# Optimization experiments

Hardware: AMD Instinct MI355X
Metric: run time of the kernel (lower is better)

Reference implementation:

```python
import jax, jax.numpy as jnp
import numpy as np

N = 100000
E = 1600000
F_IN = 32
HID = 16


def _sage_conv(x, src, dst, W_l, b_l, W_r):
    # PyG SAGEConv (aggr='mean', normalize=False, root_weight=True):
    #   out = lin_l(mean_{j in N(i)} x_j) + lin_r(x_i)
    # lin_l has bias, lin_r has no bias.
    n = x.shape[0]
    msg_sum = jax.ops.segment_sum(x[src], dst, num_segments=n)          # [N, d]
    deg = jax.ops.segment_sum(jnp.ones_like(dst, dtype=x.dtype), dst, num_segments=n)
    agg = msg_sum / jnp.maximum(deg, 1.0)[:, None]                      # mean, 0 for isolated nodes
    return agg @ W_l.T + b_l + x @ W_r.T


def setup_inputs() -> dict:
    key = jax.random.key(0)
    ks = jax.random.split(key, 8)
    x = jax.random.normal(ks[0], (N, F_IN), dtype=jnp.float32)
    edge_index = jax.random.randint(ks[1], (1, 2, E), 0, N, dtype=jnp.int64)
    s1 = 1.0 / np.sqrt(F_IN)
    s2 = 1.0 / np.sqrt(HID)
    W1_l = jax.random.uniform(ks[2], (HID, F_IN), jnp.float32, -s1, s1)
    b1_l = jax.random.uniform(ks[3], (HID,), jnp.float32, -s1, s1)
    W1_r = jax.random.uniform(ks[4], (HID, F_IN), jnp.float32, -s1, s1)
    W2_l = jax.random.uniform(ks[5], (F_IN, HID), jnp.float32, -s2, s2)
    b2_l = jax.random.uniform(ks[6], (F_IN,), jnp.float32, -s2, s2)
    W2_r = jax.random.uniform(ks[7], (F_IN, HID), jnp.float32, -s2, s2)
    return {"x": x, "edge_index": edge_index, "W1_l": W1_l, "b1_l": b1_l,
            "W1_r": W1_r, "W2_l": W2_l, "b2_l": b2_l, "W2_r": W2_r}


def reference(x, edge_index, W1_l, b1_l, W1_r, W2_l, b2_l, W2_r):
    ei = jnp.squeeze(edge_index, axis=0)  # [2, E]
    src, dst = ei[0], ei[1]
    h = jax.nn.relu(_sage_conv(x, src, dst, W1_l, b1_l, W1_r))
    out = _sage_conv(h, src, dst, W2_l, b2_l, W2_r)
    return out
```

## Files before the change

### kernel.cpp

```cpp
#include <hip/hip_runtime.h>

#define F_IN 32
#define HID 16
#define BSHIFT 6
#define BNODES (1 << BSHIFT)
#define CAP 1440
#define NBINS 2048
#define CHUNK 8192
#define SRCM 0x1FFFFu
#define WS2 17

__device__ __forceinline__ void add4(float4& a, const float4& b) {
    a.x += b.x; a.y += b.y; a.z += b.z; a.w += b.w;
}
__device__ __forceinline__ unsigned pack2(float a, float b) {
    unsigned ua = __float_as_uint(a);
    unsigned ub = __float_as_uint(b);
    ua = (ua + 0x7FFFu + ((ua >> 16) & 1u)) >> 16;
    ub = (ub + 0x7FFFu + ((ub >> 16) & 1u)) >> 16;
    return ua | (ub << 16);
}
__device__ __forceinline__ float lo2f(unsigned u) { return __uint_as_float(u << 16); }
__device__ __forceinline__ float hi2f(unsigned u) { return __uint_as_float(u & 0xFFFF0000u); }
__device__ __forceinline__ float4 unp(uint2 v) {
    return make_float4(lo2f(v.x), hi2f(v.x), lo2f(v.y), hi2f(v.y));
}

__global__ void __launch_bounds__(256) k_pre(const float* __restrict__ x,
                                             const float* __restrict__ W1_l,
                                             const float* __restrict__ b1,
                                             const float* __restrict__ W1_r,
                                             unsigned* __restrict__ y1b,
                                             float* __restrict__ y1r,
                                             const int* __restrict__ ei,
                                             int* __restrict__ bucketCursor,
                                             unsigned* __restrict__ bucketBuf,
                                             int N, int E, int nodeBlocks) {
    __shared__ int cnt[NBINS];
    __shared__ int runBase[NBINS];
    __shared__ float Wa[HID * F_IN];
    __shared__ float Wb[HID * F_IN];
    __shared__ float bb[HID];
    int tid = threadIdx.x;

    if ((int)blockIdx.x < nodeBlocks) {
        for (int i = tid; i < HID * F_IN; i += 256) { Wa[i] = W1_l[i]; Wb[i] = W1_r[i]; }
        if (tid < HID) bb[tid] = b1[tid];
        __syncthreads();
        int node = blockIdx.x * 256 + tid;
        if (node >= N) return;
        float xr[F_IN];
        const float4* xp = (const float4*)(x + (size_t)node * F_IN);
#pragma unroll
        for (int i = 0; i < F_IN / 4; i++) {
            float4 v = xp[i];
            xr[4 * i + 0] = v.x; xr[4 * i + 1] = v.y;
            xr[4 * i + 2] = v.z; xr[4 * i + 3] = v.w;
        }
        float a[HID];
#pragma unroll
        for (int o = 0; o < HID; o++) {
            float s = 0.f;
#pragma unroll
            for (int k = 0; k < F_IN; k++) s += xr[k] * Wa[o * F_IN + k];
            a[o] = s;
        }
        uint4* yp = (uint4*)(y1b + (size_t)node * 8);
        yp[0] = make_uint4(pack2(a[0], a[1]), pack2(a[2], a[3]),
                           pack2(a[4], a[5]), pack2(a[6], a[7]));
        yp[1] = make_uint4(pack2(a[8], a[9]), pack2(a[10], a[11]),
                           pack2(a[12], a[13]), pack2(a[14], a[15]));
#pragma unroll
        for (int o = 0; o < HID; o++) {
            float s = bb[o];
#pragma unroll
            for (int k = 0; k < F_IN; k++) s += xr[k] * Wb[o * F_IN + k];
            a[o] = s;
        }
        float4* rp = (float4*)(y1r + (size_t)node * HID);
        rp[0] = make_float4(a[0], a[1], a[2], a[3]);
        rp[1] = make_float4(a[4], a[5], a[6], a[7]);
        rp[2] = make_float4(a[8], a[9], a[10], a[11]);
        rp[3] = make_float4(a[12], a[13], a[14], a[15]);
        return;
    }

    int pb = blockIdx.x - nodeBlocks;
    int e0 = pb * CHUNK;
    int e1 = min(e0 + CHUNK, E);
    int n4 = (e1 - e0) >> 2;
    const int4* dst4 = (const int4*)(ei + E + e0);
    const int4* src4 = (const int4*)(ei + e0);

#pragma unroll
    for (int i = 0; i < NBINS / 256; i++) cnt[tid + 256 * i] = 0;
    __syncthreads();
    for (int i = tid; i < n4; i += 256) {
        int4 d = dst4[i];
        atomicAdd(&cnt[d.x >> BSHIFT], 1);
        atomicAdd(&cnt[d.y >> BSHIFT], 1);
        atomicAdd(&cnt[d.z >> BSHIFT], 1);
        atomicAdd(&cnt[d.w >> BSHIFT], 1);
    }
    __syncthreads();
#pragma unroll
    for (int i = 0; i < NBINS / 256; i++) {
        int b = tid + 256 * i;
        int c = cnt[b];
        runBase[b] = c ? atomicAdd(&bucketCursor[b], c) : 0;
        cnt[b] = 0;
    }
    __syncthreads();
    for (int i = tid; i < n4; i += 256) {
        int4 d = dst4[i];
        int4 s = src4[i];
        {
            int b = d.x >> BSHIFT;
            int pos = runBase[b] + atomicAdd(&cnt[b], 1);
            if (pos < CAP)
                bucketBuf[(size_t)b * CAP + pos] = ((unsigned)(d.x & (BNODES - 1)) << 17) | (unsigned)s.x;
        }
        {
            int b = d.y >> BSHIFT;
            int pos = runBase[b] + atomicAdd(&cnt[b], 1);
            if (pos < CAP)
                bucketBuf[(size_t)b * CAP + pos] = ((unsigned)(d.y & (BNODES - 1)) << 17) | (unsigned)s.y;
        }
        {
            int b = d.z >> BSHIFT;
            int pos = runBase[b] + atomicAdd(&cnt[b], 1);
            if (pos < CAP)
                bucketBuf[(size_t)b * CAP + pos] = ((unsigned)(d.z & (BNODES - 1)) << 17) | (unsigned)s.z;
        }
        {
            int b = d.w >> BSHIFT;
            int pos = runBase[b] + atomicAdd(&cnt[b], 1);
            if (pos < CAP)
                bucketBuf[(size_t)b * CAP + pos] = ((unsigned)(d.w & (BNODES - 1)) << 17) | (unsigned)s.w;
        }
    }
}

__global__ void __launch_bounds__(256) k_agg1f(const unsigned* __restrict__ y1b,
                                               const float* __restrict__ y1r,
                                               unsigned* __restrict__ bucketBuf,
                                               const int* __restrict__ bucketCursor,
                                               unsigned* __restrict__ hb,
                                               int* __restrict__ meta, int N) {
    __shared__ __align__(16) unsigned sA[CAP];
    __shared__ __align__(16) unsigned sB[CAP];
    __shared__ int hist[BNODES];
    __shared__ int scn[BNODES];
    __shared__ int cur[BNODES];
    int tid = threadIdx.x, b = blockIdx.x;

    if (tid < BNODES) hist[tid] = 0;
    int nRec = min(bucketCursor[b], CAP);
    unsigned* buf = bucketBuf + (size_t)b * CAP;
    int n4s = (nRec + 3) >> 2;
    for (int i = tid; i < n4s; i += 256)
        ((uint4*)sA)[i] = ((const uint4*)buf)[i];
    __syncthreads();
    for (int i = tid; i < nRec; i += 256) atomicAdd(&hist[sA[i] >> 17], 1);
    __syncthreads();
    if (tid < BNODES) scn[tid] = hist[tid];
    __syncthreads();
    for (int off = 1; off < BNODES; off <<= 1) {
        int v = (tid < BNODES && tid >= off) ? scn[tid - off] : 0;
        __syncthreads();
        if (tid < BNODES && tid >= off) scn[tid] += v;
        __syncthreads();
    }
    if (tid < BNODES) cur[tid] = scn[tid] - hist[tid];
    __syncthreads();
    for (int i = tid; i < nRec; i += 256) {
        unsigned r = sA[i];
        int pos = atomicAdd(&cur[r >> 17], 1);
        sB[pos] = r & SRCM;
    }
    __syncthreads();

    for (int i = tid; i < n4s; i += 256)
        ((uint4*)buf)[i] = ((const uint4*)sB)[i];
    if (tid < BNODES) {
        meta[(size_t)b * 128 + tid] = scn[tid] - hist[tid];
        meta[(size_t)b * 128 + BNODES + tid] = scn[tid];
    }

    const uint2* yv = (const uint2*)y1b;
    {
        int nl = tid >> 2, c = tid & 3;
        int node = b * BNODES + nl;
        if (node < N) {
            int start = scn[nl] - hist[nl];
            int dg = hist[nl];
            int jend = start + dg;
            float4 a0 = make_float4(0, 0, 0, 0), a1 = a0;
            int j = start;
            for (; j + 4 <= jend; j += 4) {
                unsigned s0 = sB[j], s1 = sB[j + 1], s2 = sB[j + 2], s3 = sB[j + 3];
                uint2 v0 = yv[(size_t)s0 * 4 + c];
                uint2 v1 = yv[(size_t)s1 * 4 + c];
                uint2 v2 = yv[(size_t)s2 * 4 + c];
                uint2 v3 = yv[(size_t)s3 * 4 + c];
                add4(a0, unp(v0)); add4(a1, unp(v1));
                add4(a0, unp(v2)); add4(a1, unp(v3));
            }
            for (; j < jend; j++) {
                uint2 v = yv[(size_t)sB[j] * 4 + c];
                add4(a0, unp(v));
            }
            add4(a0, a1);
            float inv = 1.0f / (float)(dg > 0 ? dg : 1);
            float4 r4 = ((const float4*)(y1r + (size_t)node * HID))[c];
            float o0 = fmaxf(a0.x * inv + r4.x, 0.0f);
            float o1 = fmaxf(a0.y * inv + r4.y, 0.0f);
            float o2 = fmaxf(a0.z * inv + r4.z, 0.0f);
            float o3 = fmaxf(a0.w * inv + r4.w, 0.0f);
            ((uint2*)hb)[(size_t)node * 4 + c] = make_uint2(pack2(o0, o1), pack2(o2, o3));
        }
    }
}

__global__ void __launch_bounds__(256) k_l2f(const unsigned* __restrict__ hb,
                                             const unsigned* __restrict__ bucketBuf,
                                             const int* __restrict__ bucketCursor,
                                             const int* __restrict__ meta,
                                             const float* __restrict__ W2_l,
                                             const float* __restrict__ b2,
                                             const float* __restrict__ W2_r,
                                             float* __restrict__ out, int N) {
    __shared__ __align__(16) unsigned sB[CAP];
    __shared__ int s0[BNODES];
    __shared__ int s1[BNODES];
    __shared__ float mm[BNODES * (HID + 1)];
    __shared__ float Wl[F_IN * WS2];
    __shared__ float Wr[F_IN * WS2];
    __shared__ float bs[F_IN];
    int tid = threadIdx.x, b = blockIdx.x;

    for (int i = tid; i < F_IN * HID; i += 256) {
        int r = i >> 4, q = i & 15;
        Wl[r * WS2 + q] = W2_l[i];
        Wr[r * WS2 + q] = W2_r[i];
    }
    if (tid < F_IN) bs[tid] = b2[tid];
    if (tid < BNODES) {
        s0[tid] = meta[(size_t)b * 128 + tid];
        s1[tid] = meta[(size_t)b * 128 + BNODES + tid];
    }
    int nRec = min(bucketCursor[b], CAP);
    const uint4* bv = (const uint4*)(bucketBuf + (size_t)b * CAP);
    int n4s = (nRec + 3) >> 2;
    for (int i = tid; i < n4s; i += 256) ((uint4*)sB)[i] = bv[i];
    __syncthreads();

    const uint2* hv = (const uint2*)hb;
    {
        int nl = tid >> 2, c = tid & 3;
        int node = b * BNODES + nl;
        if (node < N) {
            int start = s0[nl];
            int jend = s1[nl];
            int dg = jend - start;
            float4 a0 = make_float4(0, 0, 0, 0), a1 = a0;
            int j = start;
            for (; j + 4 <= jend; j += 4) {
                unsigned v0i = sB[j], v1i = sB[j + 1], v2i = sB[j + 2], v3i = sB[j + 3];
                uint2 v0 = hv[(size_t)v0i * 4 + c];
                uint2 v1 = hv[(size_t)v1i * 4 + c];
                uint2 v2 = hv[(size_t)v2i * 4 + c];
                uint2 v3 = hv[(size_t)v3i * 4 + c];
                add4(a0, unp(v0)); add4(a1, unp(v1));
                add4(a0, unp(v2)); add4(a1, unp(v3));
            }
            for (; j < jend; j++) {
                uint2 v = hv[(size_t)sB[j] * 4 + c];
                add4(a0, unp(v));
            }
            add4(a0, a1);
            float inv = 1.0f / (float)(dg > 0 ? dg : 1);
            mm[nl * (HID + 1) + c * 4 + 0] = a0.x * inv;
            mm[nl * (HID + 1) + c * 4 + 1] = a0.y * inv;
            mm[nl * (HID + 1) + c * 4 + 2] = a0.z * inv;
            mm[nl * (HID + 1) + c * 4 + 3] = a0.w * inv;
        }
    }
    __syncthreads();

    {
        int nl = tid >> 2, c = tid & 3;
        int node = b * BNODES + nl;
        if (node >= N) return;

        float m[HID];
#pragma unroll
        for (int k = 0; k < HID; k++) m[k] = mm[nl * (HID + 1) + k];

        float hr[HID];
        const uint4* hp = (const uint4*)(hb + (size_t)node * 8);
        uint4 u0 = hp[0], u1 = hp[1];
        hr[0] = lo2f(u0.x); hr[1] = hi2f(u0.x); hr[2] = lo2f(u0.y); hr[3] = hi2f(u0.y);
        hr[4] = lo2f(u0.z); hr[5] = hi2f(u0.z); hr[6] = lo2f(u0.w); hr[7] = hi2f(u0.w);
        hr[8] = lo2f(u1.x); hr[9] = hi2f(u1.x); hr[10] = lo2f(u1.y); hr[11] = hi2f(u1.y);
        hr[12] = lo2f(u1.z); hr[13] = hi2f(u1.z); hr[14] = lo2f(u1.w); hr[15] = hi2f(u1.w);

        float a[8];
#pragma unroll
        for (int jj = 0; jj < 8; jj++) {
            int o = c * 8 + jj;
            float s = bs[o];
#pragma unroll
            for (int k = 0; k < HID; k++)
                s += m[k] * Wl[o * WS2 + k] + hr[k] * Wr[o * WS2 + k];
            a[jj] = s;
        }
        float4* op = (float4*)(out + (size_t)node * F_IN + c * 8);
        op[0] = make_float4(a[0], a[1], a[2], a[3]);
        op[1] = make_float4(a[4], a[5], a[6], a[7]);
    }
}

extern "C" void kernel_launch(void* const* d_in, const int* in_sizes, int n_in,
                              void* d_out, int out_size, void* d_ws, size_t ws_size,
                              hipStream_t stream) {
    const float* x    = (const float*)d_in[0];
    const int*   ei   = (const int*)d_in[1];
    const float* W1_l = (const float*)d_in[2];
    const float* b1   = (const float*)d_in[3];
    const float* W1_r = (const float*)d_in[4];
    const float* W2_l = (const float*)d_in[5];
    const float* b2   = (const float*)d_in[6];
    const float* W2_r = (const float*)d_in[7];
    float* out = (float*)d_out;

    const int N = in_sizes[0] / F_IN;
    const int E = in_sizes[1] / 2;
    const int nbuckets = (N + BNODES - 1) >> BSHIFT;

    int* bucketCursor = (int*)d_ws;
    unsigned* bucketBuf = (unsigned*)(bucketCursor + NBINS);
    unsigned* y1b = bucketBuf + (size_t)nbuckets * CAP;
    unsigned* hb  = y1b + (size_t)N * 8;
    int* meta = (int*)(hb + (size_t)N * 8);
    float* y1r = (float*)(meta + (size_t)nbuckets * 128);

    hipMemsetAsync(bucketCursor, 0, NBINS * sizeof(int), stream);

    const int nodeBlocks = (N + 255) / 256;
    const int partBlocks = (E + CHUNK - 1) / CHUNK;

    k_pre<<<nodeBlocks + partBlocks, 256, 0, stream>>>(x, W1_l, b1, W1_r,
                                                       y1b, y1r, ei,
                                                       bucketCursor, bucketBuf,
                                                       N, E, nodeBlocks);
    k_agg1f<<<nbuckets, 256, 0, stream>>>(y1b, y1r, bucketBuf, bucketCursor,
                                          hb, meta, N);
    k_l2f<<<nbuckets, 256, 0, stream>>>(hb, bucketBuf, bucketCursor, meta,
                                        W2_l, b2, W2_r, out, N);
}
```

Before: 147.3 us.

## Replace shared-memory binning with direct global atomics per edge in bucketing pass

```diff
diff --git a/kernel.cpp b/kernel.cpp
--- a/kernel.cpp
+++ b/kernel.cpp
@@ -6,7 +6,7 @@
 #define BNODES (1 << BSHIFT)
 #define CAP 1440
 #define NBINS 2048
-#define CHUNK 8192
+#define CHUNK 2048
 #define SRCM 0x1FFFFu
 #define WS2 17
 
@@ -36,14 +36,12 @@
                                              int* __restrict__ bucketCursor,
                                              unsigned* __restrict__ bucketBuf,
                                              int N, int E, int nodeBlocks) {
-    __shared__ int cnt[NBINS];
-    __shared__ int runBase[NBINS];
-    __shared__ float Wa[HID * F_IN];
-    __shared__ float Wb[HID * F_IN];
-    __shared__ float bb[HID];
     int tid = threadIdx.x;
 
     if ((int)blockIdx.x < nodeBlocks) {
+        __shared__ float Wa[HID * F_IN];
+        __shared__ float Wb[HID * F_IN];
+        __shared__ float bb[HID];
         for (int i = tid; i < HID * F_IN; i += 256) { Wa[i] = W1_l[i]; Wb[i] = W1_r[i]; }
         if (tid < HID) bb[tid] = b1[tid];
         __syncthreads();
@@ -92,52 +90,23 @@
     const int4* dst4 = (const int4*)(ei + E + e0);
     const int4* src4 = (const int4*)(ei + e0);
 
-#pragma unroll
-    for (int i = 0; i < NBINS / 256; i++) cnt[tid + 256 * i] = 0;
-    __syncthreads();
-    for (int i = tid; i < n4; i += 256) {
-        int4 d = dst4[i];
-        atomicAdd(&cnt[d.x >> BSHIFT], 1);
-        atomicAdd(&cnt[d.y >> BSHIFT], 1);
-        atomicAdd(&cnt[d.z >> BSHIFT], 1);
-        atomicAdd(&cnt[d.w >> BSHIFT], 1);
-    }
-    __syncthreads();
-#pragma unroll
-    for (int i = 0; i < NBINS / 256; i++) {
-        int b = tid + 256 * i;
-        int c = cnt[b];
-        runBase[b] = c ? atomicAdd(&bucketCursor[b], c) : 0;
-        cnt[b] = 0;
-    }
-    __syncthreads();
     for (int i = tid; i < n4; i += 256) {
         int4 d = dst4[i];
         int4 s = src4[i];
-        {
-            int b = d.x >> BSHIFT;
-            int pos = runBase[b] + atomicAdd(&cnt[b], 1);
-            if (pos < CAP)
-                bucketBuf[(size_t)b * CAP + pos] = ((unsigned)(d.x & (BNODES - 1)) << 17) | (unsigned)s.x;
-        }
-        {
-            int b = d.y >> BSHIFT;
-            int pos = runBase[b] + atomicAdd(&cnt[b], 1);
-            if (pos < CAP)
-                bucketBuf[(size_t)b * CAP + pos] = ((unsigned)(d.y & (BNODES - 1)) << 17) | (unsigned)s.y;
-        }
-        {
-            int b = d.z >> BSHIFT;
-            int pos = runBase[b] + atomicAdd(&cnt[b], 1);
-            if (pos < CAP)
-                bucketBuf[(size_t)b * CAP + pos] = ((unsigned)(d.z & (BNODES - 1)) << 17) | (unsigned)s.z;
-        }
-        {
-            int b = d.w >> BSHIFT;
-            int pos = runBase[b] + atomicAdd(&cnt[b], 1);
-            if (pos < CAP)
-                bucketBuf[(size_t)b * CAP + pos] = ((unsigned)(d.w & (BNODES - 1)) << 17) | (unsigned)s.w;
-        }
+        int b0 = d.x >> BSHIFT, b1_ = d.y >> BSHIFT;
+        int b2_ = d.z >> BSHIFT, b3 = d.w >> BSHIFT;
+        int p0 = atomicAdd(&bucketCursor[b0], 1);
+        int p1 = atomicAdd(&bucketCursor[b1_], 1);
+        int p2 = atomicAdd(&bucketCursor[b2_], 1);
+        int p3 = atomicAdd(&bucketCursor[b3], 1);
+        if (p0 < CAP)
+            bucketBuf[(size_t)b0 * CAP + p0] = ((unsigned)(d.x & (BNODES - 1)) << 17) | (unsigned)s.x;
+        if (p1 < CAP)
+            bucketBuf[(size_t)b1_ * CAP + p1] = ((unsigned)(d.y & (BNODES - 1)) << 17) | (unsigned)s.y;
+        if (p2 < CAP)
+            bucketBuf[(size_t)b2_ * CAP + p2] = ((unsigned)(d.z & (BNODES - 1)) << 17) | (unsigned)s.z;
+        if (p3 < CAP)
+            bucketBuf[(size_t)b3 * CAP + p3] = ((unsigned)(d.w & (BNODES - 1)) << 17) | (unsigned)s.w;
     }
 }
 
```

Measured after the change: 362.9 us. 146% more time.

## Double bucket size to 128 nodes and gather 16-byte rows with 2 threads per node

Applied to the files above, without the earlier changes.

```diff
diff --git a/kernel.cpp b/kernel.cpp
--- a/kernel.cpp
+++ b/kernel.cpp
@@ -2,10 +2,10 @@
 
 #define F_IN 32
 #define HID 16
-#define BSHIFT 6
+#define BSHIFT 7
 #define BNODES (1 << BSHIFT)
-#define CAP 1440
-#define NBINS 2048
+#define CAP 2560
+#define NBINS 1024
 #define CHUNK 8192
 #define SRCM 0x1FFFFu
 #define WS2 17
@@ -22,8 +22,11 @@
 }
 __device__ __forceinline__ float lo2f(unsigned u) { return __uint_as_float(u << 16); }
 __device__ __forceinline__ float hi2f(unsigned u) { return __uint_as_float(u & 0xFFFF0000u); }
-__device__ __forceinline__ float4 unp(uint2 v) {
+__device__ __forceinline__ float4 unpLo(uint4 v) {
     return make_float4(lo2f(v.x), hi2f(v.x), lo2f(v.y), hi2f(v.y));
+}
+__device__ __forceinline__ float4 unpHi(uint4 v) {
+    return make_float4(lo2f(v.z), hi2f(v.z), lo2f(v.w), hi2f(v.w));
 }
 
 __global__ void __launch_bounds__(256) k_pre(const float* __restrict__ x,
@@ -183,41 +186,46 @@
     for (int i = tid; i < n4s; i += 256)
         ((uint4*)buf)[i] = ((const uint4*)sB)[i];
     if (tid < BNODES) {
-        meta[(size_t)b * 128 + tid] = scn[tid] - hist[tid];
-        meta[(size_t)b * 128 + BNODES + tid] = scn[tid];
-    }
-
-    const uint2* yv = (const uint2*)y1b;
+        meta[(size_t)b * 256 + tid] = scn[tid] - hist[tid];
+        meta[(size_t)b * 256 + BNODES + tid] = scn[tid];
+    }
+
+    const uint4* yv = (const uint4*)y1b;
     {
-        int nl = tid >> 2, c = tid & 3;
+        int nl = tid >> 1, c = tid & 1;
         int node = b * BNODES + nl;
         if (node < N) {
             int start = scn[nl] - hist[nl];
             int dg = hist[nl];
             int jend = start + dg;
             float4 a0 = make_float4(0, 0, 0, 0), a1 = a0;
+            float4 c0 = a0, c1 = a0;
             int j = start;
-            for (; j + 4 <= jend; j += 4) {
-                unsigned s0 = sB[j], s1 = sB[j + 1], s2 = sB[j + 2], s3 = sB[j + 3];
-                uint2 v0 = yv[(size_t)s0 * 4 + c];
-                uint2 v1 = yv[(size_t)s1 * 4 + c];
-                uint2 v2 = yv[(size_t)s2 * 4 + c];
-                uint2 v3 = yv[(size_t)s3 * 4 + c];
-                add4(a0, unp(v0)); add4(a1, unp(v1));
-                add4(a0, unp(v2)); add4(a1, unp(v3));
+            for (; j + 2 <= jend; j += 2) {
+                unsigned s0 = sB[j], s1 = sB[j + 1];
+                uint4 v0 = yv[(size_t)s0 * 2 + c];
+                uint4 v1 = yv[(size_t)s1 * 2 + c];
+                add4(a0, unpLo(v0)); add4(a1, unpHi(v0));
+                add4(c0, unpLo(v1)); add4(c1, unpHi(v1));
             }
-            for (; j < jend; j++) {
-                uint2 v = yv[(size_t)sB[j] * 4 + c];
-                add4(a0, unp(v));
+            if (j < jend) {
+                uint4 v = yv[(size_t)sB[j] * 2 + c];
+                add4(a0, unpLo(v)); add4(a1, unpHi(v));
             }
-            add4(a0, a1);
+            add4(a0, c0); add4(a1, c1);
             float inv = 1.0f / (float)(dg > 0 ? dg : 1);
-            float4 r4 = ((const float4*)(y1r + (size_t)node * HID))[c];
-            float o0 = fmaxf(a0.x * inv + r4.x, 0.0f);
-            float o1 = fmaxf(a0.y * inv + r4.y, 0.0f);
-            float o2 = fmaxf(a0.z * inv + r4.z, 0.0f);
-            float o3 = fmaxf(a0.w * inv + r4.w, 0.0f);
-            ((uint2*)hb)[(size_t)node * 4 + c] = make_uint2(pack2(o0, o1), pack2(o2, o3));
+            const float4* rp = (const float4*)(y1r + (size_t)node * HID);
+            float4 r0 = rp[c * 2], r1 = rp[c * 2 + 1];
+            float o0 = fmaxf(a0.x * inv + r0.x, 0.0f);
+            float o1 = fmaxf(a0.y * inv + r0.y, 0.0f);
+            float o2 = fmaxf(a0.z * inv + r0.z, 0.0f);
+            float o3 = fmaxf(a0.w * inv + r0.w, 0.0f);
+            float o4 = fmaxf(a1.x * inv + r1.x, 0.0f);
+            float o5 = fmaxf(a1.y * inv + r1.y, 0.0f);
+            float o6 = fmaxf(a1.z * inv + r1.z, 0.0f);
+            float o7 = fmaxf(a1.w * inv + r1.w, 0.0f);
+            ((uint4*)hb)[(size_t)node * 2 + c] =
+                make_uint4(pack2(o0, o1), pack2(o2, o3), pack2(o4, o5), pack2(o6, o7));
         }
     }
 }
@@ -246,8 +254,8 @@
     }
     if (tid < F_IN) bs[tid] = b2[tid];
     if (tid < BNODES) {
-        s0[tid] = meta[(size_t)b * 128 + tid];
-        s1[tid] = meta[(size_t)b * 128 + BNODES + tid];
+        s0[tid] = meta[(size_t)b * 256 + tid];
+        s1[tid] = meta[(size_t)b * 256 + BNODES + tid];
     }
     int nRec = min(bucketCursor[b], CAP);
     const uint4* bv = (const uint4*)(bucketBuf + (size_t)b * CAP);
@@ -255,70 +263,64 @@
     for (int i = tid; i < n4s; i += 256) ((uint4*)sB)[i] = bv[i];
     __syncthreads();
 
-    const uint2* hv = (const uint2*)hb;
-    {
-        int nl = tid >> 2, c = tid & 3;
-        int node = b * BNODES + nl;
-        if (node < N) {
-            int start = s0[nl];
-            int jend = s1[nl];
-            int dg = jend - start;
-            float4 a0 = make_float4(0, 0, 0, 0), a1 = a0;
-            int j = start;
-            for (; j + 4 <= jend; j += 4) {
-                unsigned v0i = sB[j], v1i = sB[j + 1], v2i = sB[j + 2], v3i = sB[j + 3];
-                uint2 v0 = hv[(size_t)v0i * 4 + c];
-                uint2 v1 = hv[(size_t)v1i * 4 + c];
-                uint2 v2 = hv[(size_t)v2i * 4 + c];
-                uint2 v3 = hv[(size_t)v3i * 4 + c];
-                add4(a0, unp(v0)); add4(a1, unp(v1));
-                add4(a0, unp(v2)); add4(a1, unp(v3));
-            }
-            for (; j < jend; j++) {
-                uint2 v = hv[(size_t)sB[j] * 4 + c];
-                add4(a0, unp(v));
-            }
-            add4(a0, a1);
-            float inv = 1.0f / (float)(dg > 0 ? dg : 1);
-            mm[nl * (HID + 1) + c * 4 + 0] = a0.x * inv;
-            mm[nl * (HID + 1) + c * 4 + 1] = a0.y * inv;
-            mm[nl * (HID + 1) + c * 4 + 2] = a0.z * inv;
-            mm[nl * (HID + 1) + c * 4 + 3] = a0.w * inv;
-        }
-    }
-    __syncthreads();
-
-    {
-        int nl = tid >> 2, c = tid & 3;
-        int node = b * BNODES + nl;
-        if (node >= N) return;
-
-        float m[HID];
-#pragma unroll
-        for (int k = 0; k < HID; k++) m[k] = mm[nl * (HID + 1) + k];
-
-        float hr[HID];
-        const uint4* hp = (const uint4*)(hb + (size_t)node * 8);
-        uint4 u0 = hp[0], u1 = hp[1];
-        hr[0] = lo2f(u0.x); hr[1] = hi2f(u0.x); hr[2] = lo2f(u0.y); hr[3] = hi2f(u0.y);
-        hr[4] = lo2f(u0.z); hr[5] = hi2f(u0.z); hr[6] = lo2f(u0.w); hr[7] = hi2f(u0.w);
-        hr[8] = lo2f(u1.x); hr[9] = hi2f(u1.x); hr[10] = lo2f(u1.y); hr[11] = hi2f(u1.y);
-        hr[12] = lo2f(u1.z); hr[13] = hi2f(u1.z); hr[14] = lo2f(u1.w); hr[15] = hi2f(u1.w);
-
-        float a[8];
-#pragma unroll
-        for (int jj = 0; jj < 8; jj++) {
-            int o = c * 8 + jj;
-            float s = bs[o];
-#pragma unroll
-            for (int k = 0; k < HID; k++)
-                s += m[k] * Wl[o * WS2 + k] + hr[k] * Wr[o * WS2 + k];
-            a[jj] = s;
-        }
-        float4* op = (float4*)(out + (size_t)node * F_IN + c * 8);
-        op[0] = make_float4(a[0], a[1], a[2], a[3]);
-        op[1] = make_float4(a[4], a[5], a[6], a[7]);
-    }
+    const uint4* hv = (const uint4*)hb;
+    int nl = tid >> 1, c = tid & 1;
+    int node = b * BNODES + nl;
+    if (node < N) {
+        int start = s0[nl];
+        int jend = s1[nl];
+        int dg = jend - start;
+        float4 a0 = make_float4(0, 0, 0, 0), a1 = a0;
+        float4 c0 = a0, c1 = a0;
+        int j = start;
+        for (; j + 2 <= jend; j += 2) {
+            unsigned v0i = sB[j], v1i = sB[j + 1];
+            uint4 v0 = hv[(size_t)v0i * 2 + c];
+            uint4 v1 = hv[(size_t)v1i * 2 + c];
+            add4(a0, unpLo(v0)); add4(a1, unpHi(v0));
+            add4(c0, unpLo(v1)); add4(c1, unpHi(v1));
+        }
+        if (j < jend) {
+            uint4 v = hv[(size_t)sB[j] * 2 + c];
+            add4(a0, unpLo(v)); add4(a1, unpHi(v));
+        }
+        add4(a0, c0); add4(a1, c1);
+        float inv = 1.0f / (float)(dg > 0 ? dg : 1);
+        float* mp = mm + nl * (HID + 1) + c * 8;
+        mp[0] = a0.x * inv; mp[1] = a0.y * inv; mp[2] = a0.z * inv; mp[3] = a0.w * inv;
+        mp[4] = a1.x * inv; mp[5] = a1.y * inv; mp[6] = a1.z * inv; mp[7] = a1.w * inv;
+    }
+    __syncthreads();
+
+    if (node >= N) return;
+
+    float m[HID];
+#pragma unroll
+    for (int k = 0; k < HID; k++) m[k] = mm[nl * (HID + 1) + k];
+
+    float hr[HID];
+    const uint4* hp = (const uint4*)(hb + (size_t)node * 8);
+    uint4 u0 = hp[0], u1 = hp[1];
+    hr[0] = lo2f(u0.x); hr[1] = hi2f(u0.x); hr[2] = lo2f(u0.y); hr[3] = hi2f(u0.y);
+    hr[4] = lo2f(u0.z); hr[5] = hi2f(u0.z); hr[6] = lo2f(u0.w); hr[7] = hi2f(u0.w);
+    hr[8] = lo2f(u1.x); hr[9] = hi2f(u1.x); hr[10] = lo2f(u1.y); hr[11] = hi2f(u1.y);
+    hr[12] = lo2f(u1.z); hr[13] = hi2f(u1.z); hr[14] = lo2f(u1.w); hr[15] = hi2f(u1.w);
+
+    float a[16];
+#pragma unroll
+    for (int jj = 0; jj < 16; jj++) {
+        int o = c * 16 + jj;
+        float s = bs[o];
+#pragma unroll
+        for (int k = 0; k < HID; k++)
+            s += m[k] * Wl[o * WS2 + k] + hr[k] * Wr[o * WS2 + k];
+        a[jj] = s;
+    }
+    float4* op = (float4*)(out + (size_t)node * F_IN + c * 16);
+    op[0] = make_float4(a[0], a[1], a[2], a[3]);
+    op[1] = make_float4(a[4], a[5], a[6], a[7]);
+    op[2] = make_float4(a[8], a[9], a[10], a[11]);
+    op[3] = make_float4(a[12], a[13], a[14], a[15]);
 }
 
 extern "C" void kernel_launch(void* const* d_in, const int* in_sizes, int n_in,
@@ -343,7 +345,7 @@
     unsigned* y1b = bucketBuf + (size_t)nbuckets * CAP;
     unsigned* hb  = y1b + (size_t)N * 8;
     int* meta = (int*)(hb + (size_t)N * 8);
-    float* y1r = (float*)(meta + (size_t)nbuckets * 128);
+    float* y1r = (float*)(meta + (size_t)nbuckets * 256);
 
     hipMemsetAsync(bucketCursor, 0, NBINS * sizeof(int), stream);
 
```

New measurement: 151.2 us. +2.6%, slower.
